# Kernel optimization log

Hardware: AMD Instinct MI355X
Metric: run time of the kernel (lower is better)

Reference implementation:

```python
import jax, jax.numpy as jnp
import numpy as np
import math

INPUT_SIZE = 128  # feature dim D, from init_kwargs

def setup_inputs() -> dict:
    key = jax.random.key(0)
    k1, k2 = jax.random.split(key)
    B, N, D = 4, 4096, INPUT_SIZE
    inp = jax.random.normal(k1, (B, N, D), dtype=jnp.float32)
    adj = jax.random.randint(k2, (B, N, N), 0, 2, dtype=jnp.int32)
    return {"input": inp, "adj": adj}

def reference(input, adj):
    # scores: [B, N, N] = X X^T / sqrt(D)
    scores = jnp.matmul(input, jnp.swapaxes(input, 1, 2)) / math.sqrt(INPUT_SIZE)
    neg = jnp.asarray(-1e12, dtype=scores.dtype)
    masked = jnp.where(adj > 0, scores, neg)
    attention = jax.nn.softmax(masked, axis=2)
    out_hid = jnp.matmul(attention, input)  # [B, N, D]
    return out_hid
```

## Files before the change

### kernel.cpp

```cpp
#include <hip/hip_runtime.h>
#include <hip/hip_bf16.h>


#define NN 4096
#define DD 128
#define BK 128
#define NT (NN / BK)

#define XBT_REL 32768
#define BUF1_OFF 65536
#define P_OFF 131072
#define P_WSTRIDE 1280
#define LDS_BYTES (P_OFF + 16 * P_WSTRIDE)

typedef __attribute__((ext_vector_type(8))) short bf16x8;
typedef __attribute__((ext_vector_type(4))) float f32x4;

static __device__ __forceinline__ unsigned f2bf(float f) {
    union { float f; unsigned u; } v; v.f = f;
    return (v.u + 0x7fffu + ((v.u >> 16) & 1u)) >> 16;
}

static __device__ __forceinline__ void gl_lds16(const void* g, void* l) {
    __builtin_amdgcn_global_load_lds(
        (const __attribute__((address_space(1))) unsigned*)g,
        (__attribute__((address_space(3))) unsigned*)l, 16, 0, 0);
}

__global__ __launch_bounds__(256)
void gat_prep(const float* __restrict__ X, unsigned short* __restrict__ xb,
              unsigned short* __restrict__ xbt) {
    __shared__ unsigned short tile[64][132];
    const int t = threadIdx.x;
    const int b  = blockIdx.x >> 6;
    const int kc = blockIdx.x & 63;
    const float* src = X + ((size_t)b * NN + kc * 64) * DD;
    unsigned short* xbo = xb + ((size_t)b * NN + kc * 64) * DD;

    #pragma unroll
    for (int it = 0; it < 8; ++it) {
        int f = it * 256 + t;
        int k = f >> 5, d4 = (f & 31) * 4;
        float4 v = *(const float4*)(src + (size_t)f * 4);
        uint2 pk;
        pk.x = f2bf(v.x) | (f2bf(v.y) << 16);
        pk.y = f2bf(v.z) | (f2bf(v.w) << 16);
        *(uint2*)(xbo + (size_t)f * 4) = pk;
        *(uint2*)(&tile[k][d4]) = pk;
    }
    __syncthreads();
    const int d = t >> 1, kb0 = (t & 1) * 32;
    unsigned short* dst = xbt + (size_t)b * DD * NN + (size_t)d * NN + kc * 64 + kb0;
    #pragma unroll
    for (int c = 0; c < 4; ++c) {
        union { uint4 o; unsigned short e[8]; } u;
        #pragma unroll
        for (int j = 0; j < 8; ++j) u.e[j] = tile[kb0 + c * 8 + j][d];
        *(uint4*)(dst + c * 8) = u.o;
    }
}

__global__ __launch_bounds__(1024, 4)
void gat_fused(const unsigned short* __restrict__ xb,
               const unsigned short* __restrict__ xbt,
               const int* __restrict__ adj,
               float* __restrict__ out) {
    extern __shared__ char lds[];
    const int t = threadIdx.x;
    const int w = t >> 6, l = t & 63;
    const int h = l >> 4, l16 = l & 15;
    const int rw = w & 3;
    const int kh = w >> 2;

    const int bid  = blockIdx.x;
    const int b    = bid >> 6;
    const int row0 = (bid & 63) * 64;
    const int qbase = row0 + rw * 16;
    const int kbase = kh * 32;

    const char* xb_b  = (const char*)(xb  + (size_t)b * NN * DD);
    const char* xbt_b = (const char*)(xbt + (size_t)b * DD * NN);
    const int*  Ag    = adj + (size_t)b * NN * NN;
    float*      Og    = out + (size_t)b * NN * DD;

    bf16x8 qfrag[4];
    {
        const char* qp = xb_b + (size_t)(qbase + l16) * DD * 2;
        #pragma unroll
        for (int ds = 0; ds < 4; ++ds)
            qfrag[ds] = *(const bf16x8*)(qp + ds * 64 + h * 16);
    }

    int off_xb[2], off_xbt[2];
    #pragma unroll
    for (int j = 0; j < 2; ++j) {
        int r0 = w * 8 + 4 * j + h;
        off_xb[j]  = r0 * 256      + ((l16 ^ (r0 & 7)) * 16);
        off_xbt[j] = r0 * (NN * 2) + ((l16 ^ (r0 & 7)) * 16);
    }
    char* bufA = lds;
    char* bufB = lds + BUF1_OFF;
    char* pw   = lds + P_OFF + w * P_WSTRIDE;

    const int* arow = Ag + (size_t)(qbase + l16) * NN + kbase + 4 * h;

    #pragma unroll
    for (int j = 0; j < 2; ++j) {
        gl_lds16(xb_b  + off_xb[j],  bufA + w * 2048 + j * 1024);
        gl_lds16(xbt_b + off_xbt[j], bufA + XBT_REL + w * 2048 + j * 1024);
    }
    int4 avA0 = *(const int4*)(arow);
    int4 avA1 = *(const int4*)(arow + 16);

    f32x4 oacc[8];
    #pragma unroll
    for (int cf = 0; cf < 8; ++cf) oacc[cf] = (f32x4){0.f, 0.f, 0.f, 0.f};
    float psum = 0.f;

#define COMPUTE(BUF, AV0, AV1) do {                                            \
    f32x4 sacc0 = (f32x4){0.f,0.f,0.f,0.f}, sacc1 = (f32x4){0.f,0.f,0.f,0.f};  \
    {                                                                          \
        const int krow0 = kbase + l16;                                         \
        const int krow1 = kbase + 16 + l16;                                    \
        const char* rp0 = (BUF) + krow0 * 256;                                 \
        const char* rp1 = (BUF) + krow1 * 256;                                 \
        const int sw = l16 & 7;                                                \
        _Pragma("unroll")                                                      \
        for (int ds = 0; ds < 4; ++ds) {                                       \
            bf16x8 kf0 = *(const bf16x8*)(rp0 + (((h + 4*ds) ^ sw) * 16));     \
            sacc0 = __builtin_amdgcn_mfma_f32_16x16x32_bf16(                   \
                kf0, qfrag[ds], sacc0, 0, 0, 0);                               \
            bf16x8 kf1 = *(const bf16x8*)(rp1 + (((h + 4*ds) ^ sw) * 16));     \
            sacc1 = __builtin_amdgcn_mfma_f32_16x16x32_bf16(                   \
                kf1, qfrag[ds], sacc1, 0, 0, 0);                               \
        }                                                                      \
    }                                                                          \
    {                                                                          \
        const float SC = 0.08838834764831845f;                                 \
        float p0 = ((AV0).x > 0) ? __expf(sacc0[0] * SC) : 0.f;                \
        float p1 = ((AV0).y > 0) ? __expf(sacc0[1] * SC) : 0.f;                \
        float p2 = ((AV0).z > 0) ? __expf(sacc0[2] * SC) : 0.f;                \
        float p3 = ((AV0).w > 0) ? __expf(sacc0[3] * SC) : 0.f;                \
        psum += p0 + p1 + p2 + p3;                                             \
        uint2 pk0; pk0.x = f2bf(p0) | (f2bf(p1) << 16);                        \
        pk0.y = f2bf(p2) | (f2bf(p3) << 16);                                   \
        *(uint2*)(pw + l16 * 80 + h * 8) = pk0;                                \
        float q0 = ((AV1).x > 0) ? __expf(sacc1[0] * SC) : 0.f;                \
        float q1 = ((AV1).y > 0) ? __expf(sacc1[1] * SC) : 0.f;                \
        float q2 = ((AV1).z > 0) ? __expf(sacc1[2] * SC) : 0.f;                \
        float q3 = ((AV1).w > 0) ? __expf(sacc1[3] * SC) : 0.f;                \
        psum += q0 + q1 + q2 + q3;                                             \
        uint2 pk1; pk1.x = f2bf(q0) | (f2bf(q1) << 16);                        \
        pk1.y = f2bf(q2) | (f2bf(q3) << 16);                                   \
        *(uint2*)(pw + l16 * 80 + 32 + h * 8) = pk1;                           \
    }                                                                          \
    {                                                                          \
        bf16x8 pfrag = *(const bf16x8*)(pw + l16 * 80 + h * 16);               \
        _Pragma("unroll")                                                      \
        for (int cf = 0; cf < 8; ++cf) {                                       \
            const int vrow = l16 + 16 * cf;                                    \
            bf16x8 vfrag = *(const bf16x8*)((BUF) + XBT_REL + vrow * 256       \
                              + (((4*kh + h) ^ (vrow & 7)) * 16));             \
            oacc[cf] = __builtin_amdgcn_mfma_f32_16x16x32_bf16(                \
                pfrag, vfrag, oacc[cf], 0, 0, 0);                              \
        }                                                                      \
    }                                                                          \
} while (0)

    for (int kt = 0; kt < NT - 1; ++kt) {
        int4 avB0 = *(const int4*)(arow + (kt + 1) * BK);
        int4 avB1 = *(const int4*)(arow + (kt + 1) * BK + 16);
        asm volatile("s_waitcnt vmcnt(2)" ::: "memory");
        __builtin_amdgcn_s_barrier();
        #pragma unroll
        for (int j = 0; j < 2; ++j) {
            gl_lds16(xb_b  + (size_t)(kt + 1) * BK * 256 + off_xb[j],
                     bufB + w * 2048 + j * 1024);
            gl_lds16(xbt_b + (size_t)(kt + 1) * BK * 2 + off_xbt[j],
                     bufB + XBT_REL + w * 2048 + j * 1024);
        }
        COMPUTE(bufA, avA0, avA1);
        char* tmp = bufA; bufA = bufB; bufB = tmp;
        avA0 = avB0; avA1 = avB1;
    }
    asm volatile("s_waitcnt vmcnt(0)" ::: "memory");
    __builtin_amdgcn_s_barrier();
    COMPUTE(bufA, avA0, avA1);

    psum += __shfl_xor(psum, 16, 64);
    psum += __shfl_xor(psum, 32, 64);

    __syncthreads();
    float* psarea = (float*)(lds + P_OFF);
    if (l < 16) psarea[w * 16 + l] = psum;
    float* oa = (float*)lds;
    if (kh >= 2) {
        float* dst = oa + ((kh - 2) * 4 + rw) * 2048;
        #pragma unroll
        for (int cf = 0; cf < 8; ++cf)
            #pragma unroll
            for (int r = 0; r < 4; ++r)
                dst[(4 * h + r) * 128 + l16 + 16 * cf] = oacc[cf][r];
    }
    __syncthreads();
    if (kh < 2) {
        const float* sp = oa + (kh * 4 + rw) * 2048;
        #pragma unroll
        for (int cf = 0; cf < 8; ++cf)
            #pragma unroll
            for (int r = 0; r < 4; ++r)
                oacc[cf][r] += sp[(4 * h + r) * 128 + l16 + 16 * cf];
    }
    __syncthreads();
    if (kh == 1) {
        float* dst = oa + rw * 2048;
        #pragma unroll
        for (int cf = 0; cf < 8; ++cf)
            #pragma unroll
            for (int r = 0; r < 4; ++r)
                dst[(4 * h + r) * 128 + l16 + 16 * cf] = oacc[cf][r];
    }
    __syncthreads();
    if (kh == 0) {
        const float* sp = oa + rw * 2048;
        float inv[4];
        #pragma unroll
        for (int r = 0; r < 4; ++r) {
            int q = 4 * h + r;
            float tot = psarea[rw * 16 + q]       + psarea[(4 + rw) * 16 + q]
                      + psarea[(8 + rw) * 16 + q] + psarea[(12 + rw) * 16 + q];
            inv[r] = 1.0f / tot;
        }
        float* dst = oa + rw * 2048;
        #pragma unroll
        for (int cf = 0; cf < 8; ++cf)
            #pragma unroll
            for (int r = 0; r < 4; ++r)
                dst[(4 * h + r) * 128 + l16 + 16 * cf] =
                    (oacc[cf][r] + sp[(4 * h + r) * 128 + l16 + 16 * cf]) * inv[r];
    }
    __syncthreads();
    const float4* oaf4 = (const float4*)oa;
    float4* dstf4 = (float4*)(Og + (size_t)row0 * DD);
    dstf4[t]        = oaf4[t];
    dstf4[t + 1024] = oaf4[t + 1024];
#undef COMPUTE
}

extern "C" void kernel_launch(void* const* d_in, const int* in_sizes, int n_in,
                              void* d_out, int out_size, void* d_ws, size_t ws_size,
                              hipStream_t stream) {
    const float* X   = (const float*)d_in[0];
    const int*   adj = (const int*)d_in[1];
    float*       out = (float*)d_out;
    unsigned short* xb  = (unsigned short*)d_ws;
    unsigned short* xbt = xb + (size_t)4 * NN * DD;

    hipFuncSetAttribute((const void*)gat_fused,
                        hipFuncAttributeMaxDynamicSharedMemorySize, LDS_BYTES);
    gat_prep<<<dim3(256), dim3(256), 0, stream>>>(X, xb, xbt);
    gat_fused<<<dim3(256), dim3(1024), LDS_BYTES, stream>>>(xb, xbt, adj, out);
}
```

Measured before the change: 399.9 us.

## Switch to 32x32x16 MFMA tiles with 8 waves and simpler cross-wave reduction

Restructures the fused attention kernel so each wave computes a 32x32 score tile with the 32x32x16 bf16 MFMA instead of two 16x16x32 tiles. The block shrinks to 8 waves (2 row groups by 4 key slices), each staging twice as many rows per tile. The multi-step pairwise LDS reduction of partial outputs is replaced by one dump of all partials followed by a single-pass sum, normalize and store. This aims to cut LDS fragment traffic per MFMA flop and the epilogue barriers, at the cost of fewer waves for latency hiding and more accumulator registers.

```diff
diff --git a/kernel.cpp b/kernel.cpp
--- a/kernel.cpp
+++ b/kernel.cpp
@@ -10,11 +10,11 @@
 #define XBT_REL 32768
 #define BUF1_OFF 65536
 #define P_OFF 131072
-#define P_WSTRIDE 1280
-#define LDS_BYTES (P_OFF + 16 * P_WSTRIDE)
+#define P_WSTRIDE 2304
+#define LDS_BYTES (P_OFF + 8 * P_WSTRIDE)
 
 typedef __attribute__((ext_vector_type(8))) short bf16x8;
-typedef __attribute__((ext_vector_type(4))) float f32x4;
+typedef __attribute__((ext_vector_type(16))) float f32x16;
 
 static __device__ __forceinline__ unsigned f2bf(float f) {
     union { float f; unsigned u; } v; v.f = f;
@@ -60,7 +60,7 @@
     }
 }
 
-__global__ __launch_bounds__(1024, 4)
+__global__ __launch_bounds__(512, 2)
 void gat_fused(const unsigned short* __restrict__ xb,
                const unsigned short* __restrict__ xbt,
                const int* __restrict__ adj,
@@ -68,14 +68,13 @@
     extern __shared__ char lds[];
     const int t = threadIdx.x;
     const int w = t >> 6, l = t & 63;
-    const int h = l >> 4, l16 = l & 15;
-    const int rw = w & 3;
-    const int kh = w >> 2;
-
+    const int l32 = l & 31, h5 = l >> 5;
+    const int rw = w >> 2;
+    const int kh = w & 3;
     const int bid  = blockIdx.x;
     const int b    = bid >> 6;
     const int row0 = (bid & 63) * 64;
-    const int qbase = row0 + rw * 16;
+    const int qbase = row0 + rw * 32;
     const int kbase = kh * 32;
 
     const char* xb_b  = (const char*)(xb  + (size_t)b * NN * DD);
@@ -83,168 +82,159 @@
     const int*  Ag    = adj + (size_t)b * NN * NN;
     float*      Og    = out + (size_t)b * NN * DD;
 
-    bf16x8 qfrag[4];
+    bf16x8 qfrag[8];
     {
-        const char* qp = xb_b + (size_t)(qbase + l16) * DD * 2;
-        #pragma unroll
-        for (int ds = 0; ds < 4; ++ds)
-            qfrag[ds] = *(const bf16x8*)(qp + ds * 64 + h * 16);
-    }
-
-    int off_xb[2], off_xbt[2];
-    #pragma unroll
-    for (int j = 0; j < 2; ++j) {
-        int r0 = w * 8 + 4 * j + h;
-        off_xb[j]  = r0 * 256      + ((l16 ^ (r0 & 7)) * 16);
-        off_xbt[j] = r0 * (NN * 2) + ((l16 ^ (r0 & 7)) * 16);
+        const char* qp = xb_b + (size_t)(qbase + l32) * 256;
+        #pragma unroll
+        for (int c = 0; c < 8; ++c)
+            qfrag[c] = *(const bf16x8*)(qp + c * 32 + h5 * 16);
+    }
+
+    int off_xb[4], off_xbt[4];
+    #pragma unroll
+    for (int j = 0; j < 4; ++j) {
+        int r = w * 16 + 4 * j + (l >> 4);
+        off_xb[j]  = r * 256      + (((l & 15) ^ (r & 7)) * 16);
+        off_xbt[j] = r * (NN * 2) + (((l & 15) ^ (r & 7)) * 16);
     }
     char* bufA = lds;
     char* bufB = lds + BUF1_OFF;
     char* pw   = lds + P_OFF + w * P_WSTRIDE;
-
-    const int* arow = Ag + (size_t)(qbase + l16) * NN + kbase + 4 * h;
-
-    #pragma unroll
-    for (int j = 0; j < 2; ++j) {
-        gl_lds16(xb_b  + off_xb[j],  bufA + w * 2048 + j * 1024);
-        gl_lds16(xbt_b + off_xbt[j], bufA + XBT_REL + w * 2048 + j * 1024);
-    }
-    int4 avA0 = *(const int4*)(arow);
-    int4 avA1 = *(const int4*)(arow + 16);
-
-    f32x4 oacc[8];
-    #pragma unroll
-    for (int cf = 0; cf < 8; ++cf) oacc[cf] = (f32x4){0.f, 0.f, 0.f, 0.f};
+    const int* arow = Ag + (size_t)(qbase + l32) * NN + kbase + 4 * h5;
+
+#define STAGE(BUF, KEY0) do {                                                  \
+    _Pragma("unroll")                                                          \
+    for (int j = 0; j < 4; ++j) {                                              \
+        gl_lds16(xb_b  + (size_t)(KEY0) * 256 + off_xb[j],                     \
+                 (BUF) + w * 4096 + j * 1024);                                 \
+        gl_lds16(xbt_b + (size_t)(KEY0) * 2 + off_xbt[j],                      \
+                 (BUF) + XBT_REL + w * 4096 + j * 1024);                       \
+    }                                                                          \
+} while (0)
+
+    STAGE(bufA, 0);
+    int4 avA[4];
+    #pragma unroll
+    for (int g = 0; g < 4; ++g) avA[g] = *(const int4*)(arow + g * 8);
+
+    f32x16 oacc[4];
+    #pragma unroll
+    for (int d = 0; d < 4; ++d) oacc[d] = (f32x16)(0.0f);
     float psum = 0.f;
 
-#define COMPUTE(BUF, AV0, AV1) do {                                            \
-    f32x4 sacc0 = (f32x4){0.f,0.f,0.f,0.f}, sacc1 = (f32x4){0.f,0.f,0.f,0.f};  \
+#define COMPUTE(BUF, AV) do {                                                  \
+    f32x16 sacc = (f32x16)(0.0f);                                              \
     {                                                                          \
-        const int krow0 = kbase + l16;                                         \
-        const int krow1 = kbase + 16 + l16;                                    \
-        const char* rp0 = (BUF) + krow0 * 256;                                 \
-        const char* rp1 = (BUF) + krow1 * 256;                                 \
-        const int sw = l16 & 7;                                                \
+        const int krow = kbase + l32;                                          \
+        const char* kp = (BUF) + krow * 256;                                   \
+        const int sw = krow & 7;                                               \
         _Pragma("unroll")                                                      \
-        for (int ds = 0; ds < 4; ++ds) {                                       \
-            bf16x8 kf0 = *(const bf16x8*)(rp0 + (((h + 4*ds) ^ sw) * 16));     \
-            sacc0 = __builtin_amdgcn_mfma_f32_16x16x32_bf16(                   \
-                kf0, qfrag[ds], sacc0, 0, 0, 0);                               \
-            bf16x8 kf1 = *(const bf16x8*)(rp1 + (((h + 4*ds) ^ sw) * 16));     \
-            sacc1 = __builtin_amdgcn_mfma_f32_16x16x32_bf16(                   \
-                kf1, qfrag[ds], sacc1, 0, 0, 0);                               \
+        for (int c = 0; c < 8; ++c) {                                          \
+            bf16x8 kf = *(const bf16x8*)(kp + (((2 * c + h5) ^ sw) * 16));     \
+            sacc = __builtin_amdgcn_mfma_f32_32x32x16_bf16(                    \
+                kf, qfrag[c], sacc, 0, 0, 0);                                  \
         }                                                                      \
     }                                                                          \
     {                                                                          \
-        const float SC = 0.08838834764831845f;                                 \
-        float p0 = ((AV0).x > 0) ? __expf(sacc0[0] * SC) : 0.f;                \
-        float p1 = ((AV0).y > 0) ? __expf(sacc0[1] * SC) : 0.f;                \
-        float p2 = ((AV0).z > 0) ? __expf(sacc0[2] * SC) : 0.f;                \
-        float p3 = ((AV0).w > 0) ? __expf(sacc0[3] * SC) : 0.f;                \
-        psum += p0 + p1 + p2 + p3;                                             \
-        uint2 pk0; pk0.x = f2bf(p0) | (f2bf(p1) << 16);                        \
-        pk0.y = f2bf(p2) | (f2bf(p3) << 16);                                   \
-        *(uint2*)(pw + l16 * 80 + h * 8) = pk0;                                \
-        float q0 = ((AV1).x > 0) ? __expf(sacc1[0] * SC) : 0.f;                \
-        float q1 = ((AV1).y > 0) ? __expf(sacc1[1] * SC) : 0.f;                \
-        float q2 = ((AV1).z > 0) ? __expf(sacc1[2] * SC) : 0.f;                \
-        float q3 = ((AV1).w > 0) ? __expf(sacc1[3] * SC) : 0.f;                \
-        psum += q0 + q1 + q2 + q3;                                             \
-        uint2 pk1; pk1.x = f2bf(q0) | (f2bf(q1) << 16);                        \
-        pk1.y = f2bf(q2) | (f2bf(q3) << 16);                                   \
-        *(uint2*)(pw + l16 * 80 + 32 + h * 8) = pk1;                           \
+        const float SC = 0.08838834764831845f;                \
+        _Pragma("unroll")                                                      \
+        for (int g = 0; g < 4; ++g) {                                          \
+            int4 a = (AV)[g];                                                  \
+            float p0 = (a.x > 0) ? __expf(sacc[4 * g + 0] * SC) : 0.f;         \
+            float p1 = (a.y > 0) ? __expf(sacc[4 * g + 1] * SC) : 0.f;         \
+            float p2 = (a.z > 0) ? __expf(sacc[4 * g + 2] * SC) : 0.f;         \
+            float p3 = (a.w > 0) ? __expf(sacc[4 * g + 3] * SC) : 0.f;         \
+            psum += p0 + p1 + p2 + p3;                                         \
+            uint2 pk;                                                          \
+            pk.x = f2bf(p0) | (f2bf(p1) << 16);                                \
+            pk.y = f2bf(p2) | (f2bf(p3) << 16);                                \
+            *(uint2*)(pw + l32 * 72 + g * 16 + h5 * 8) = pk;                   \
+        }                                                                      \
     }                                                                          \
     {                                                                          \
-        bf16x8 pfrag = *(const bf16x8*)(pw + l16 * 80 + h * 16);               \
+        bf16x8 pf0 = *(const bf16x8*)(pw + l32 * 72 + h5 * 16);                \
+        bf16x8 pf1 = *(const bf16x8*)(pw + l32 * 72 + 32 + h5 * 16);           \
         _Pragma("unroll")                                                      \
-        for (int cf = 0; cf < 8; ++cf) {                                       \
-            const int vrow = l16 + 16 * cf;                                    \
-            bf16x8 vfrag = *(const bf16x8*)((BUF) + XBT_REL + vrow * 256       \
-                              + (((4*kh + h) ^ (vrow & 7)) * 16));             \
-            oacc[cf] = __builtin_amdgcn_mfma_f32_16x16x32_bf16(                \
-                pfrag, vfrag, oacc[cf], 0, 0, 0);                              \
+        for (int db = 0; db < 4; ++db) {                                       \
+            const int vrow = db * 32 + l32;                                    \
+            const int swv = vrow & 7;                                          \
+            const char* vp = (BUF) + XBT_REL + vrow * 256;                     \
+            bf16x8 v0 = *(const bf16x8*)(vp + (((4 * kh + h5) ^ swv) * 16));   \
+            oacc[db] = __builtin_amdgcn_mfma_f32_32x32x16_bf16(                \
+                pf0, v0, oacc[db], 0, 0, 0);                                   \
+            bf16x8 v1 = *(const bf16x8*)(vp + (((4 * kh + 2 + h5) ^ swv) * 16)); \
+            oacc[db] = __builtin_amdgcn_mfma_f32_32x32x16_bf16(                \
+                pf1, v1, oacc[db], 0, 0, 0);                                   \
         }                                                                      \
     }                                                                          \
 } while (0)
 
     for (int kt = 0; kt < NT - 1; ++kt) {
-        int4 avB0 = *(const int4*)(arow + (kt + 1) * BK);
-        int4 avB1 = *(const int4*)(arow + (kt + 1) * BK + 16);
-        asm volatile("s_waitcnt vmcnt(2)" ::: "memory");
+        int4 avB[4];
+        #pragma unroll
+        for (int g = 0; g < 4; ++g)
+            avB[g] = *(const int4*)(arow + (kt + 1) * BK + g * 8);
+        asm volatile("s_waitcnt vmcnt(4)" ::: "memory");
         __builtin_amdgcn_s_barrier();
-        #pragma unroll
-        for (int j = 0; j < 2; ++j) {
-            gl_lds16(xb_b  + (size_t)(kt + 1) * BK * 256 + off_xb[j],
-                     bufB + w * 2048 + j * 1024);
-            gl_lds16(xbt_b + (size_t)(kt + 1) * BK * 2 + off_xbt[j],
-                     bufB + XBT_REL + w * 2048 + j * 1024);
-        }
-        COMPUTE(bufA, avA0, avA1);
+        STAGE(bufB, (kt + 1) * BK);
+        COMPUTE(bufA, avA);
         char* tmp = bufA; bufA = bufB; bufB = tmp;
-        avA0 = avB0; avA1 = avB1;
+        #pragma unroll
+        for (int g = 0; g < 4; ++g) avA[g] = avB[g];
     }
     asm volatile("s_waitcnt vmcnt(0)" ::: "memory");
     __builtin_amdgcn_s_barrier();
-    COMPUTE(bufA, avA0, avA1);
-
-    psum += __shfl_xor(psum, 16, 64);
+    COMPUTE(bufA, avA);
+
     psum += __shfl_xor(psum, 32, 64);
-
     __syncthreads();
-    float* psarea = (float*)(lds + P_OFF);
-    if (l < 16) psarea[w * 16 + l] = psum;
-    float* oa = (float*)lds;
-    if (kh >= 2) {
-        float* dst = oa + ((kh - 2) * 4 + rw) * 2048;
-        #pragma unroll
-        for (int cf = 0; cf < 8; ++cf)
+
+    float* slot = (float*)(lds + w * 17408);
+    #pragma unroll
+    for (int db = 0; db < 4; ++db)
+        #pragma unroll
+        for (int r = 0; r < 16; ++r) {
+            const int lrow = (r & 3) + 8 * (r >> 2) + 4 * h5;
+            slot[lrow * 136 + db * 32 + l32] = oacc[db][r];
+        }
+    float* psarea = (float*)(lds + 139264);
+    if (l < 32) psarea[w * 32 + l] = psum;
+    __syncthreads();
+
+    {
+        const int R   = w * 8 + (l >> 3);
+        const int q32 = R & 31, rwR = R >> 5;
+        const int d0  = (l & 7) * 16;
+        float tot = psarea[(rwR * 4 + 0) * 32 + q32]
+                  + psarea[(rwR * 4 + 1) * 32 + q32]
+                  + psarea[(rwR * 4 + 2) * 32 + q32]
+                  + psarea[(rwR * 4 + 3) * 32 + q32];
+        float invt = 1.0f / tot;
+        float4 acc[4];
+        #pragma unroll
+        for (int j = 0; j < 4; ++j) acc[j] = (float4){0.f, 0.f, 0.f, 0.f};
+        #pragma unroll
+        for (int kx = 0; kx < 4; ++kx) {
+            const float* sp = (const float*)(lds + (rwR * 4 + kx) * 17408)
+                              + q32 * 136 + d0;
             #pragma unroll
-            for (int r = 0; r < 4; ++r)
-                dst[(4 * h + r) * 128 + l16 + 16 * cf] = oacc[cf][r];
-    }
-    __syncthreads();
-    if (kh < 2) {
-        const float* sp = oa + (kh * 4 + rw) * 2048;
-        #pragma unroll
-        for (int cf = 0; cf < 8; ++cf)
-            #pragma unroll
-            for (int r = 0; r < 4; ++r)
-                oacc[cf][r] += sp[(4 * h + r) * 128 + l16 + 16 * cf];
-    }
-    __syncthreads();
-    if (kh == 1) {
-        float* dst = oa + rw * 2048;
-        #pragma unroll
-        for (int cf = 0; cf < 8; ++cf)
-            #pragma unroll
-            for (int r = 0; r < 4; ++r)
-                dst[(4 * h + r) * 128 + l16 + 16 * cf] = oacc[cf][r];
-    }
-    __syncthreads();
-    if (kh == 0) {
-        const float* sp = oa + rw * 2048;
-        float inv[4];
-        #pragma unroll
-        for (int r = 0; r < 4; ++r) {
-            int q = 4 * h + r;
-            float tot = psarea[rw * 16 + q]       + psarea[(4 + rw) * 16 + q]
-                      + psarea[(8 + rw) * 16 + q] + psarea[(12 + rw) * 16 + q];
-            inv[r] = 1.0f / tot;
+            for (int j = 0; j < 4; ++j) {
+                float4 v = *(const float4*)(sp + 4 * j);
+                acc[j].x += v.x; acc[j].y += v.y;
+                acc[j].z += v.z; acc[j].w += v.w;
+            }
         }
-        float* dst = oa + rw * 2048;
-        #pragma unroll
-        for (int cf = 0; cf < 8; ++cf)
-            #pragma unroll
-            for (int r = 0; r < 4; ++r)
-                dst[(4 * h + r) * 128 + l16 + 16 * cf] =
-                    (oacc[cf][r] + sp[(4 * h + r) * 128 + l16 + 16 * cf]) * inv[r];
-    }
-    __syncthreads();
-    const float4* oaf4 = (const float4*)oa;
-    float4* dstf4 = (float4*)(Og + (size_t)row0 * DD);
-    dstf4[t]        = oaf4[t];
-    dstf4[t + 1024] = oaf4[t + 1024];
+        float* op = Og + (size_t)(row0 + R) * DD + d0;
+        #pragma unroll
+        for (int j = 0; j < 4; ++j) {
+            float4 res;
+            res.x = acc[j].x * invt; res.y = acc[j].y * invt;
+            res.z = acc[j].z * invt; res.w = acc[j].w * invt;
+            *(float4*)(op + 4 * j) = res;
+        }
+    }
 #undef COMPUTE
+#undef STAGE
 }
 
 extern "C" void kernel_launch(void* const* d_in, const int* in_sizes, int n_in,
@@ -259,5 +249,5 @@
     hipFuncSetAttribute((const void*)gat_fused,
                         hipFuncAttributeMaxDynamicSharedMemorySize, LDS_BYTES);
     gat_prep<<<dim3(256), dim3(256), 0, stream>>>(X, xb, xbt);
-    gat_fused<<<dim3(256), dim3(1024), LDS_BYTES, stream>>>(xb, xbt, adj, out);
-}
+    gat_fused<<<dim3(256), dim3(512), LDS_BYTES, stream>>>(xb, xbt, adj, out);
+}
```

Result: slower. 415.4 us (+3.9%).
